# Optimization experiments

Hardware: AMD Instinct MI355X
Metric: run time of the kernel (lower is better)

The kernel has to match this reference:

```python
import jax, jax.numpy as jnp
import numpy as np
import math

B_SZ, T_LEN = 2, 1024
D_MODEL, D_STATE, D_CONV, EXPAND = 1024, 16, 4, 2
D_INNER = EXPAND * D_MODEL            # 2048
DT_RANK = math.ceil(D_MODEL / 16)     # 64


def setup_inputs() -> dict:
    key = jax.random.key(0)
    ks = jax.random.split(key, 10)
    f32 = jnp.float32
    x = jax.random.normal(ks[0], (B_SZ, T_LEN, D_MODEL), f32)
    norm_w = jnp.ones((D_MODEL,), f32)
    in_proj_w = jax.random.normal(ks[1], (2 * D_INNER, D_MODEL), f32) / np.sqrt(D_MODEL)
    conv_w = jax.random.uniform(ks[2], (D_INNER, 1, D_CONV), f32, -0.5, 0.5)
    conv_b = jax.random.uniform(ks[3], (D_INNER,), f32, -0.5, 0.5)
    x_proj_w = jax.random.normal(ks[4], (DT_RANK + 2 * D_STATE, D_INNER), f32) / np.sqrt(D_INNER)
    dt_std = DT_RANK ** (-0.5)
    dt_proj_w = jax.random.uniform(ks[5], (D_INNER, DT_RANK), f32, -dt_std, dt_std)
    # dt bias init: softplus(bias) lands in [dt_min, dt_max]
    dt = jnp.exp(jax.random.uniform(ks[6], (D_INNER,), f32) * (np.log(0.1) - np.log(0.001)) + np.log(0.001))
    dt_proj_b = dt + jnp.log(-jnp.expm1(-dt))
    A_log = jnp.log(jnp.tile(jnp.arange(1, D_STATE + 1, dtype=f32)[None, :], (D_INNER, 1)))
    D_param = jnp.ones((D_INNER,), f32)
    out_proj_w = jax.random.normal(ks[7], (D_MODEL, D_INNER), f32) / np.sqrt(D_INNER)
    return {"x": x, "norm_w": norm_w, "in_proj_w": in_proj_w, "conv_w": conv_w,
            "conv_b": conv_b, "x_proj_w": x_proj_w, "dt_proj_w": dt_proj_w,
            "dt_proj_b": dt_proj_b, "A_log": A_log, "D_param": D_param,
            "out_proj_w": out_proj_w}


def _mamba_forward(x, norm_w, in_proj_w, conv_w, conv_b, x_proj_w,
                   dt_proj_w, dt_proj_b, A_log, D_param, out_proj_w):
    residual = x
    # RMSNorm (torch nn.RMSNorm, eps=None -> finfo eps)
    eps = jnp.finfo(x.dtype).eps
    xn = x * jax.lax.rsqrt(jnp.mean(x * x, axis=-1, keepdims=True) + eps) * norm_w
    # input projection -> ssm stream + gate
    xz = xn @ in_proj_w.T                     # [B,T,2*d_inner]
    x_s, z = xz[..., :D_INNER], xz[..., D_INNER:]
    # causal depthwise conv1d (pad left d_conv-1, matches padding=d_conv-1 then [:T])
    u = jax.lax.conv_general_dilated(
        x_s.transpose(0, 2, 1), conv_w, window_strides=(1,),
        padding=[(D_CONV - 1, 0)], dimension_numbers=("NCH", "OIH", "NCH"),
        feature_group_count=D_INNER) + conv_b[None, :, None]
    u = jax.nn.silu(u).transpose(0, 2, 1)     # [B,T,d_inner]
    # input-dependent SSM params
    x_dbc = u @ x_proj_w.T
    dt_raw = x_dbc[..., :DT_RANK]
    B_ssm = x_dbc[..., DT_RANK:DT_RANK + D_STATE]
    C_ssm = x_dbc[..., DT_RANK + D_STATE:]
    delta = jax.nn.softplus(dt_raw @ dt_proj_w.T + dt_proj_b)   # [B,T,d_inner]
    A = -jnp.exp(A_log)                                         # [d_inner,d_state]
    # discretize
    dA = jnp.exp(jnp.einsum("bti,is->btis", delta, A))          # [B,T,i,s]
    dBu = jnp.einsum("bti,bts->btis", delta * u, B_ssm)         # [B,T,i,s]
    # sequential scan over time (lax.scan, carry h [B,i,s])
    def step(h, inp):
        dA_t, dBu_t, C_t = inp
        h = dA_t * h + dBu_t
        y_t = jnp.einsum("bis,bs->bi", h, C_t)
        return h, y_t
    h0 = jnp.zeros((x.shape[0], D_INNER, D_STATE), x.dtype)
    _, ys = jax.lax.scan(step, h0,
                         (dA.transpose(1, 0, 2, 3), dBu.transpose(1, 0, 2, 3),
                          C_ssm.transpose(1, 0, 2)))
    y = ys.transpose(1, 0, 2) + u * D_param                     # [B,T,d_inner]
    y = y * jax.nn.silu(z)
    return y @ out_proj_w.T + residual


def reference(x, norm_w, in_proj_w, conv_w, conv_b, x_proj_w,
              dt_proj_w, dt_proj_b, A_log, D_param, out_proj_w):
    return _mamba_forward(x, norm_w, in_proj_w, conv_w, conv_b, x_proj_w,
                          dt_proj_w, dt_proj_b, A_log, D_param, out_proj_w)
```

## Files before the change

kernel.cpp:

```cpp
#include <hip/hip_runtime.h>
#include <math.h>

#define B_SZ 2
#define T_LEN 1024
#define D_MODEL 1024
#define D_STATE 16
#define D_INNER 2048
#define DT_RANK 64
#define NTOK (B_SZ * T_LEN)
#define XPROJ_OUT 96
#define XPROJ_LD 128
#define NCHUNK 32
#define CHUNK_L (T_LEN / NCHUNK)
#define NSPLIT 16

typedef __attribute__((ext_vector_type(8))) short bf16x8;
typedef __attribute__((ext_vector_type(4))) float f32x4;

__device__ __forceinline__ float sigmoidf_(float x) { return 1.f / (1.f + __expf(-x)); }

__device__ __forceinline__ unsigned f2bf_u(float f) {
    unsigned u = __float_as_uint(f);
    return (u + 0x7FFFu + ((u >> 16) & 1u)) >> 16;
}
__device__ __forceinline__ float bf2f(unsigned short u) {
    return __uint_as_float((unsigned)u << 16);
}

__device__ __forceinline__ void gload_lds16(const void* g, void* l) {
    __builtin_amdgcn_global_load_lds((const __attribute__((address_space(1))) unsigned*)g,
                                     (__attribute__((address_space(3))) unsigned*)l,
                                     16, 0, 0);
}

__global__ __launch_bounds__(256) void k_prep(const float* __restrict__ x,
                                              const float* __restrict__ norm_w,
                                              const float* __restrict__ w_in,
                                              const float* __restrict__ w_out,
                                              const float* __restrict__ w_x,
                                              const float* __restrict__ w_dt,
                                              unsigned short* __restrict__ xn,
                                              unsigned* __restrict__ wib,
                                              unsigned* __restrict__ wob,
                                              unsigned* __restrict__ wxb,
                                              unsigned* __restrict__ wdtb) {
    __shared__ float red[4];
    int blk = blockIdx.x;
    if (blk < 2048) {
        const float* xr = x + (size_t)blk * D_MODEL;
        int i = threadIdx.x * 4;
        float4 xv = *(const float4*)(xr + i);
        float s = xv.x * xv.x + xv.y * xv.y + xv.z * xv.z + xv.w * xv.w;
#pragma unroll
        for (int m = 1; m <= 32; m <<= 1) s += __shfl_xor(s, m);
        if ((threadIdx.x & 63) == 0) red[threadIdx.x >> 6] = s;
        __syncthreads();
        float tot = red[0] + red[1] + red[2] + red[3];
        float scale = rsqrtf(tot * (1.f / D_MODEL) + 1.1920929e-07f);
        float4 wv = *(const float4*)(norm_w + i);
        uint2 o;
        o.x = f2bf_u(xv.x * scale * wv.x) | (f2bf_u(xv.y * scale * wv.y) << 16);
        o.y = f2bf_u(xv.z * scale * wv.z) | (f2bf_u(xv.w * scale * wv.w) << 16);
        *(uint2*)(xn + (size_t)blk * D_MODEL + i) = o;
        return;
    }
    blk -= 2048;
    const float* src;
    unsigned* dst;
    int lidx;
    if (blk < 2048) {
        src = w_in; dst = wib; lidx = blk * 256 + threadIdx.x;
    } else if (blk < 3072) {
        src = w_out; dst = wob; lidx = (blk - 2048) * 256 + threadIdx.x;
    } else if (blk < 3200) {
        dst = wxb; lidx = (blk - 3072) * 256 + threadIdx.x;
        if (lidx * 8 >= 96 * 2048) {
            uint4 z = {0, 0, 0, 0};
            ((uint4*)dst)[lidx] = z;
            return;
        }
        src = w_x;
    } else {
        src = w_dt; dst = wdtb; lidx = (blk - 3200) * 256 + threadIdx.x;
    }
    float4 a = ((const float4*)src)[lidx * 2];
    float4 b = ((const float4*)src)[lidx * 2 + 1];
    uint4 o;
    o.x = f2bf_u(a.x) | (f2bf_u(a.y) << 16);
    o.y = f2bf_u(a.z) | (f2bf_u(a.w) << 16);
    o.z = f2bf_u(b.x) | (f2bf_u(b.y) << 16);
    o.w = f2bf_u(b.z) | (f2bf_u(b.w) << 16);
    ((uint4*)dst)[lidx] = o;
}


template <int BN, int CW, int EPI>
__global__ __launch_bounds__(256) void gemm_bf16(const unsigned short* __restrict__ A,
                                                 const unsigned short* __restrict__ B,
                                                 void* __restrict__ Cv, int ldc, int K,
                                                 const float* __restrict__ res) {
    constexpr int RW = 4 / CW;
    constexpr int MI = (128 / RW) / 16;
    constexpr int NJ = (BN / CW) / 16;
    __shared__ __align__(16) unsigned short smem[2 * 128 * 64 + 2 * BN * 64];
    unsigned short* As0 = smem;
    unsigned short* Bs0 = smem + 2 * 128 * 64;
    int tid = threadIdx.x;
    int lane = tid & 63, wv = tid >> 6;
    int wr = wv / CW, wc = wv % CW;
    int lm = lane & 15, q = lane >> 4;
    int sw = lm & 7;
    int m0 = blockIdx.x * 128, n0 = blockIdx.y * BN;
    f32x4 acc[MI][NJ] = {};

    auto stage = [&](int bufi, int k0) {
#pragma unroll
        for (int it = 0; it < 4; ++it) {
            int chunk = it * 256 + tid;
            int cc = (chunk & 7) ^ ((chunk >> 3) & 7);
            const unsigned short* g = A + (size_t)(m0 + (chunk >> 3)) * K + k0 + cc * 8;
            char* l = (char*)(As0 + bufi * 128 * 64) + (it * 256 + wv * 64) * 16 + lane * 16;
            gload_lds16(g, l);
        }
#pragma unroll
        for (int it = 0; it < BN / 32; ++it) {
            int chunk = it * 256 + tid;
            int cc = (chunk & 7) ^ ((chunk >> 3) & 7);
            const unsigned short* g = B + (size_t)(n0 + (chunk >> 3)) * K + k0 + cc * 8;
            char* l = (char*)(Bs0 + bufi * BN * 64) + (it * 256 + wv * 64) * 16 + lane * 16;
            gload_lds16(g, l);
        }
    };

    stage(0, 0);
    __syncthreads();
    int cur = 0;
    for (int k0 = 0; k0 < K; k0 += 64) {
        if (k0 + 64 < K) stage(cur ^ 1, k0 + 64);
        const unsigned short* Ac = As0 + cur * 128 * 64;
        const unsigned short* Bc = Bs0 + cur * BN * 64;
#pragma unroll
        for (int h = 0; h < 2; ++h) {
            bf16x8 af[MI], bfr[NJ];
#pragma unroll
            for (int i = 0; i < MI; ++i)
                af[i] = *(const bf16x8*)(Ac + (wr * MI * 16 + i * 16 + lm) * 64 +
                                         (((h << 2) + q) ^ sw) * 8);
#pragma unroll
            for (int j = 0; j < NJ; ++j)
                bfr[j] = *(const bf16x8*)(Bc + (wc * NJ * 16 + j * 16 + lm) * 64 +
                                          (((h << 2) + q) ^ sw) * 8);
#pragma unroll
            for (int i = 0; i < MI; ++i)
#pragma unroll
                for (int j = 0; j < NJ; ++j)
                    acc[i][j] = __builtin_amdgcn_mfma_f32_16x16x32_bf16(af[i], bfr[j], acc[i][j], 0, 0, 0);
        }
        __syncthreads();
        cur ^= 1;
    }
    if (EPI == 0) {
        constexpr int LDT = BN + 8;
        float* Ct = (float*)smem;
#pragma unroll
        for (int i = 0; i < MI; ++i)
#pragma unroll
            for (int j = 0; j < NJ; ++j)
#pragma unroll
                for (int r = 0; r < 4; ++r) {
                    int lr = wr * MI * 16 + i * 16 + q * 4 + r;
                    int lc = wc * NJ * 16 + j * 16 + lm;
                    Ct[lr * LDT + lc] = acc[i][j][r];
                }
        __syncthreads();
        int r0 = tid >> 4, c4 = (tid & 15) * 4;
#pragma unroll
        for (int rr = 0; rr < 8; ++rr) {
            int lr = r0 + rr * 16;
            float4 v = *(float4*)&Ct[lr * LDT + c4];
            float4 rv = *(const float4*)&res[(size_t)(m0 + lr) * ldc + n0 + c4];
            v.x += rv.x; v.y += rv.y; v.z += rv.z; v.w += rv.w;
            *(float4*)&((float*)Cv)[(size_t)(m0 + lr) * ldc + n0 + c4] = v;
        }
    } else {
        constexpr int LDT = BN + 16;
        unsigned short* Ct = smem;
#pragma unroll
        for (int i = 0; i < MI; ++i)
#pragma unroll
            for (int j = 0; j < NJ; ++j)
#pragma unroll
                for (int r = 0; r < 4; ++r) {
                    int lr = wr * MI * 16 + i * 16 + q * 4 + r;
                    int lc = wc * NJ * 16 + j * 16 + lm;
                    float v = acc[i][j][r];
                    if (EPI == 1) {
                        v += res[n0 + lc];
                        v = (v > 20.f) ? v : __logf(1.f + __expf(v));
                    } else {
                        if (n0 >= D_INNER) v = v * sigmoidf_(v);
                    }
                    Ct[lr * LDT + lc] = (unsigned short)f2bf_u(v);
                }
        __syncthreads();
        constexpr int CW8 = BN / 8;
        constexpr int RPP = 256 / CW8;
        int r0 = tid / CW8, cc = (tid % CW8) * 8;
#pragma unroll
        for (int rr = 0; rr < 128 / RPP; ++rr) {
            int lr = r0 + rr * RPP;
            uint4 v = *(uint4*)&Ct[lr * LDT + cc];
            *(uint4*)&((unsigned short*)Cv)[(size_t)(m0 + lr) * ldc + n0 + cc] = v;
        }
    }
}

__global__ __launch_bounds__(256) void xproj_gemm(const unsigned short* __restrict__ A,
                                                  const unsigned short* __restrict__ B,
                                                  unsigned short* __restrict__ part) {
    constexpr int MI = 4, NJ = 4;
    __shared__ __align__(16) unsigned short smem[4 * 128 * 64];
    unsigned short* As0 = smem;
    unsigned short* Bs0 = smem + 2 * 128 * 64;
    int tid = threadIdx.x;
    int lane = tid & 63, wv = tid >> 6;
    int wr = wv >> 1, wc = wv & 1;
    int lm = lane & 15, q = lane >> 4;
    int sw = lm & 7;
    int m0 = blockIdx.x * 128;
    int kbase = blockIdx.y * 128;
    f32x4 acc[MI][NJ] = {};

    auto stage = [&](int bufi, int k0) {
#pragma unroll
        for (int it = 0; it < 4; ++it) {
            int chunk = it * 256 + tid;
            int cc = (chunk & 7) ^ ((chunk >> 3) & 7);
            const unsigned short* g = A + (size_t)(m0 + (chunk >> 3)) * D_INNER + k0 + cc * 8;
            char* l = (char*)(As0 + bufi * 128 * 64) + (it * 256 + wv * 64) * 16 + lane * 16;
            gload_lds16(g, l);
        }
#pragma unroll
        for (int it = 0; it < 4; ++it) {
            int chunk = it * 256 + tid;
            int cc = (chunk & 7) ^ ((chunk >> 3) & 7);
            const unsigned short* g = B + (size_t)(chunk >> 3) * D_INNER + k0 + cc * 8;
            char* l = (char*)(Bs0 + bufi * 128 * 64) + (it * 256 + wv * 64) * 16 + lane * 16;
            gload_lds16(g, l);
        }
    };

    stage(0, kbase);
    __syncthreads();
    for (int ks = 0; ks < 2; ++ks) {
        if (ks == 0) stage(1, kbase + 64);
        const unsigned short* Ac = As0 + ks * 128 * 64;
        const unsigned short* Bc = Bs0 + ks * 128 * 64;
#pragma unroll
        for (int h = 0; h < 2; ++h) {
            bf16x8 af[MI], bfr[NJ];
#pragma unroll
            for (int i = 0; i < MI; ++i)
                af[i] = *(const bf16x8*)(Ac + (wr * 64 + i * 16 + lm) * 64 + (((h << 2) + q) ^ sw) * 8);
#pragma unroll
            for (int j = 0; j < NJ; ++j)
                bfr[j] = *(const bf16x8*)(Bc + (wc * 64 + j * 16 + lm) * 64 + (((h << 2) + q) ^ sw) * 8);
#pragma unroll
            for (int i = 0; i < MI; ++i)
#pragma unroll
                for (int j = 0; j < NJ; ++j)
                    acc[i][j] = __builtin_amdgcn_mfma_f32_16x16x32_bf16(af[i], bfr[j], acc[i][j], 0, 0, 0);
        }
        __syncthreads();
    }
    constexpr int LDT = 144;
    unsigned short* Ct = smem;
#pragma unroll
    for (int i = 0; i < MI; ++i)
#pragma unroll
        for (int j = 0; j < NJ; ++j)
#pragma unroll
            for (int r = 0; r < 4; ++r) {
                int lr = wr * 64 + i * 16 + q * 4 + r;
                int lc = wc * 64 + j * 16 + lm;
                Ct[lr * LDT + lc] = (unsigned short)f2bf_u(acc[i][j][r]);
            }
    __syncthreads();
    unsigned short* dst = part + (size_t)blockIdx.y * (NTOK * XPROJ_LD);
    int r0 = tid >> 4, cc = (tid & 15) * 8;
#pragma unroll
    for (int rr = 0; rr < 8; ++rr) {
        int lr = r0 + rr * 16;
        uint4 v = *(uint4*)&Ct[lr * LDT + cc];
        *(uint4*)&dst[(size_t)(m0 + lr) * XPROJ_LD + cc] = v;
    }
}

__global__ __launch_bounds__(256) void k_xred(const unsigned short* __restrict__ part,
                                              float* __restrict__ dbc,
                                              unsigned short* __restrict__ dtrawb) {
    int idx4 = blockIdx.x * 256 + threadIdx.x;
    float s0 = 0.f, s1 = 0.f, s2 = 0.f, s3 = 0.f;
#pragma unroll
    for (int sp = 0; sp < NSPLIT; ++sp) {
        uint2 v = *(const uint2*)(part + (size_t)sp * (NTOK * XPROJ_LD) + idx4 * 4);
        s0 += __uint_as_float(v.x << 16);
        s1 += __uint_as_float(v.x & 0xFFFF0000u);
        s2 += __uint_as_float(v.y << 16);
        s3 += __uint_as_float(v.y & 0xFFFF0000u);
    }
    float4 sv = {s0, s1, s2, s3};
    *(float4*)(dbc + idx4 * 4) = sv;
    int col = (idx4 * 4) & (XPROJ_LD - 1);
    if (col < DT_RANK) {
        int row = (idx4 * 4) >> 7;
        uint2 o;
        o.x = f2bf_u(s0) | (f2bf_u(s1) << 16);
        o.y = f2bf_u(s2) | (f2bf_u(s3) << 16);
        *(uint2*)(dtrawb + (size_t)row * DT_RANK + col) = o;
    }
}

__global__ __launch_bounds__(256) void k_conv(const unsigned short* __restrict__ xz,
                                              const float* __restrict__ cw,
                                              const float* __restrict__ cb,
                                              unsigned short* __restrict__ ub) {
    int idx = blockIdx.x * 256 + threadIdx.x;
    int c4 = (idx & (D_INNER / 4 - 1)) * 4;
    int t = (idx >> 9) & (T_LEN - 1);
    int b = idx >> 19;
    const unsigned short* xs = xz + (size_t)b * T_LEN * 2 * D_INNER + c4;
    float4 w[4];
#pragma unroll
    for (int i = 0; i < 4; ++i) w[i] = ((const float4*)cw)[c4 + i];
    float4 cbv = *(const float4*)(cb + c4);
    float s[4] = {cbv.x, cbv.y, cbv.z, cbv.w};
#pragma unroll
    for (int k = 0; k < 4; ++k) {
        int tt = t - 3 + k;
        if (tt >= 0) {
            ushort4 xv = *(const ushort4*)(xs + (size_t)tt * 2 * D_INNER);
            float fx0 = bf2f(xv.x), fx1 = bf2f(xv.y), fx2 = bf2f(xv.z), fx3 = bf2f(xv.w);
            float w0 = (k == 0) ? w[0].x : (k == 1) ? w[0].y : (k == 2) ? w[0].z : w[0].w;
            float w1 = (k == 0) ? w[1].x : (k == 1) ? w[1].y : (k == 2) ? w[1].z : w[1].w;
            float w2 = (k == 0) ? w[2].x : (k == 1) ? w[2].y : (k == 2) ? w[2].z : w[2].w;
            float w3 = (k == 0) ? w[3].x : (k == 1) ? w[3].y : (k == 2) ? w[3].z : w[3].w;
            s[0] = fmaf(fx0, w0, s[0]);
            s[1] = fmaf(fx1, w1, s[1]);
            s[2] = fmaf(fx2, w2, s[2]);
            s[3] = fmaf(fx3, w3, s[3]);
        }
    }
    ushort4 o;
    o.x = (unsigned short)f2bf_u(s[0] * sigmoidf_(s[0]));
    o.y = (unsigned short)f2bf_u(s[1] * sigmoidf_(s[1]));
    o.z = (unsigned short)f2bf_u(s[2] * sigmoidf_(s[2]));
    o.w = (unsigned short)f2bf_u(s[3] * sigmoidf_(s[3]));
    *(ushort4*)(ub + (size_t)(b * T_LEN + t) * D_INNER + c4) = o;
}

__global__ __launch_bounds__(256) void k_scan1(const unsigned short* __restrict__ delta,
                                               const unsigned short* __restrict__ ub,
                                               const float* __restrict__ dbc,
                                               const float* __restrict__ A_log,
                                               float* __restrict__ Pbuf,
                                               float* __restrict__ Hbuf) {
    int tid = threadIdx.x;
    int cl = tid >> 2, sq = tid & 3;
    int c0 = blockIdx.x * 64;
    int c = c0 + cl;
    int b = blockIdx.y >> 5, chunk = blockIdx.y & 31;
    int t0 = chunk * CHUNK_L;
    __shared__ float bc[CHUNK_L][32];
    __shared__ __align__(16) unsigned short sd[CHUNK_L][64];
    __shared__ __align__(16) unsigned short su[CHUNK_L][64];
    {
        int t = tid >> 3, col = (tid & 7) * 4;
        const float* src = dbc + ((size_t)b * T_LEN + t0 + t) * XPROJ_LD + DT_RANK + col;
        *(float4*)&bc[t][col] = *(const float4*)src;
    }
    {
        int r = tid >> 3, c8 = (tid & 7) * 8;
        const unsigned short* dp0 = delta + ((size_t)b * T_LEN + t0) * D_INNER + c0;
        const unsigned short* up0 = ub + ((size_t)b * T_LEN + t0) * D_INNER + c0;
        *(uint4*)&sd[r][c8] = *(const uint4*)(dp0 + (size_t)r * D_INNER + c8);
        *(uint4*)&su[r][c8] = *(const uint4*)(up0 + (size_t)r * D_INNER + c8);
    }
    __syncthreads();
    float4 av = *(const float4*)(A_log + (size_t)c * D_STATE + sq * 4);
    float A0 = -__expf(av.x), A1 = -__expf(av.y), A2 = -__expf(av.z), A3 = -__expf(av.w);
    float h0 = 0.f, h1 = 0.f, h2 = 0.f, h3 = 0.f, sumd = 0.f;
#pragma unroll 4
    for (int t = 0; t < CHUNK_L; ++t) {
        float dv = bf2f(sd[t][cl]);
        float uv = bf2f(su[t][cl]);
        float du = dv * uv;
        sumd += dv;
        float4 Bv = *(const float4*)&bc[t][sq * 4];
        h0 = fmaf(__expf(dv * A0), h0, du * Bv.x);
        h1 = fmaf(__expf(dv * A1), h1, du * Bv.y);
        h2 = fmaf(__expf(dv * A2), h2, du * Bv.z);
        h3 = fmaf(__expf(dv * A3), h3, du * Bv.w);
    }
    size_t o = ((size_t)((b * NCHUNK + chunk) * D_INNER) + c) * 16 + sq * 4;
    float4 hv = {h0, h1, h2, h3};
    *(float4*)(Hbuf + o) = hv;
    float4 pv = {__expf(A0 * sumd), __expf(A1 * sumd), __expf(A2 * sumd), __expf(A3 * sumd)};
    *(float4*)(Pbuf + o) = pv;
}

__global__ __launch_bounds__(256) void k_scan2(const float* __restrict__ Pbuf,
                                               const float* __restrict__ Hbuf,
                                               float* __restrict__ Sbuf) {
    int idx = blockIdx.x * 256 + threadIdx.x;
    int b = idx >> 15, r = idx & 32767;
    size_t base = (size_t)b * NCHUNK * (D_INNER * 16) + r;
    float p[NCHUNK], hl[NCHUNK];
#pragma unroll
    for (int ch = 0; ch < NCHUNK; ++ch) {
        size_t o = base + (size_t)ch * (D_INNER * 16);
        p[ch] = Pbuf[o];
        hl[ch] = Hbuf[o];
    }
    float h = 0.f;
#pragma unroll
    for (int ch = 0; ch < NCHUNK; ++ch) {
        Sbuf[base + (size_t)ch * (D_INNER * 16)] = h;
        h = fmaf(p[ch], h, hl[ch]);
    }
}

__global__ __launch_bounds__(256) void k_scan3(const unsigned short* __restrict__ delta,
                                               const unsigned short* __restrict__ ub,
                                               const float* __restrict__ dbc,
                                               const unsigned short* __restrict__ xz,
                                               const float* __restrict__ A_log,
                                               const float* __restrict__ Dp,
                                               const float* __restrict__ Sbuf,
                                               unsigned short* __restrict__ yb) {
    int tid = threadIdx.x;
    int cl = tid >> 2, sq = tid & 3;
    int c0 = blockIdx.x * 64;
    int c = c0 + cl;
    int b = blockIdx.y >> 5, chunk = blockIdx.y & 31;
    int t0 = chunk * CHUNK_L;
    __shared__ float bc[CHUNK_L][32];
    __shared__ __align__(16) unsigned short sd[CHUNK_L][64];
    __shared__ __align__(16) unsigned short su[CHUNK_L][64];
    __shared__ __align__(16) unsigned short szy[CHUNK_L][64];
    {
        int t = tid >> 3, col = (tid & 7) * 4;
        const float* src = dbc + ((size_t)b * T_LEN + t0 + t) * XPROJ_LD + DT_RANK + col;
        *(float4*)&bc[t][col] = *(const float4*)src;
    }
    int r = tid >> 3, c8 = (tid & 7) * 8;
    {
        const unsigned short* dp0 = delta + ((size_t)b * T_LEN + t0) * D_INNER + c0;
        const unsigned short* up0 = ub + ((size_t)b * T_LEN + t0) * D_INNER + c0;
        const unsigned short* zp0 = xz + ((size_t)b * T_LEN + t0) * 2 * D_INNER + D_INNER + c0;
        *(uint4*)&sd[r][c8] = *(const uint4*)(dp0 + (size_t)r * D_INNER + c8);
        *(uint4*)&su[r][c8] = *(const uint4*)(up0 + (size_t)r * D_INNER + c8);
        *(uint4*)&szy[r][c8] = *(const uint4*)(zp0 + (size_t)r * 2 * D_INNER + c8);
    }
    __syncthreads();
    float4 av = *(const float4*)(A_log + (size_t)c * D_STATE + sq * 4);
    float A0 = -__expf(av.x), A1 = -__expf(av.y), A2 = -__expf(av.z), A3 = -__expf(av.w);
    float Dc = Dp[c];
    size_t ho = ((size_t)((b * NCHUNK + chunk) * D_INNER) + c) * 16 + sq * 4;
    float4 hv = *(const float4*)(Sbuf + ho);
    float h0 = hv.x, h1 = hv.y, h2 = hv.z, h3 = hv.w;
#pragma unroll 2
    for (int t = 0; t < CHUNK_L; ++t) {
        float dv = bf2f(sd[t][cl]);
        float uv = bf2f(su[t][cl]);
        float du = dv * uv;
        float4 Bv = *(const float4*)&bc[t][sq * 4];
        float4 Cv = *(const float4*)&bc[t][16 + sq * 4];
        h0 = fmaf(__expf(dv * A0), h0, du * Bv.x);
        h1 = fmaf(__expf(dv * A1), h1, du * Bv.y);
        h2 = fmaf(__expf(dv * A2), h2, du * Bv.z);
        h3 = fmaf(__expf(dv * A3), h3, du * Bv.w);
        float yp = h0 * Cv.x + h1 * Cv.y + h2 * Cv.z + h3 * Cv.w;
        yp += __shfl_xor(yp, 1);
        yp += __shfl_xor(yp, 2);
        if (sq == 0) {
            float sz = bf2f(szy[t][cl]);
            szy[t][cl] = (unsigned short)f2bf_u((yp + Dc * uv) * sz);
        }
    }
    __syncthreads();
    {
        unsigned short* yp0 = yb + ((size_t)b * T_LEN + t0) * D_INNER + c0;
        *(uint4*)(yp0 + (size_t)r * D_INNER + c8) = *(uint4*)&szy[r][c8];
    }
}

extern "C" void kernel_launch(void* const* d_in, const int* in_sizes, int n_in,
                              void* d_out, int out_size, void* d_ws, size_t ws_size,
                              hipStream_t stream) {
    const float* x         = (const float*)d_in[0];
    const float* norm_w    = (const float*)d_in[1];
    const float* in_proj_w = (const float*)d_in[2];
    const float* conv_w    = (const float*)d_in[3];
    const float* conv_b    = (const float*)d_in[4];
    const float* x_proj_w  = (const float*)d_in[5];
    const float* dt_proj_w = (const float*)d_in[6];
    const float* dt_proj_b = (const float*)d_in[7];
    const float* A_log     = (const float*)d_in[8];
    const float* D_param   = (const float*)d_in[9];
    const float* out_proj_w= (const float*)d_in[10];
    float* out = (float*)d_out;

    float* ws = (float*)d_ws;
    unsigned short* xzb    = (unsigned short*)(ws);
    unsigned short* ub     = (unsigned short*)(ws + 4194304);
    unsigned short* yb     = (unsigned short*)(ws + 6291456);
    unsigned short* partb  = (unsigned short*)(ws + 8388608);
    float*          dbc    = ws + 12582912;
    unsigned short* deltab = (unsigned short*)(ws + 12845056);
    float*          Pbuf   = ws + 14942208;
    float*          Hbuf   = ws + 17039360;
    float*          Sbuf   = ws + 19136512;
    unsigned short* wib    = (unsigned short*)(ws + 21233664);
    unsigned short* wob    = (unsigned short*)(ws + 23330816);
    unsigned short* wxb    = (unsigned short*)(ws + 24379392);
    unsigned short* wdtb   = (unsigned short*)(ws + 24510464);
    unsigned short* dtrawb = (unsigned short*)(ws + 24576000);
    unsigned short* xnb    = (unsigned short*)(ws + 24641536);

    k_prep<<<5312, 256, 0, stream>>>(x, norm_w, in_proj_w, out_proj_w, x_proj_w, dt_proj_w,
                                     xnb, (unsigned*)wib, (unsigned*)wob, (unsigned*)wxb,
                                     (unsigned*)wdtb);
    gemm_bf16<128, 2, 3><<<dim3(NTOK / 128, 4096 / 128), 256, 0, stream>>>(
        xnb, wib, xzb, 2 * D_INNER, D_MODEL, nullptr);
    k_conv<<<(NTOK * D_INNER / 4) / 256, 256, 0, stream>>>(xzb, conv_w, conv_b, ub);
    xproj_gemm<<<dim3(NTOK / 128, NSPLIT), 256, 0, stream>>>(ub, wxb, partb);
    k_xred<<<(NTOK * XPROJ_LD) / 1024, 256, 0, stream>>>(partb, dbc, dtrawb);
    gemm_bf16<64, 1, 1><<<dim3(NTOK / 128, D_INNER / 64), 256, 0, stream>>>(
        dtrawb, wdtb, deltab, D_INNER, DT_RANK, dt_proj_b);
    k_scan1<<<dim3(D_INNER / 64, B_SZ * NCHUNK), 256, 0, stream>>>(deltab, ub, dbc, A_log,
                                                                   Pbuf, Hbuf);
    k_scan2<<<(B_SZ * D_INNER * D_STATE) / 256, 256, 0, stream>>>(Pbuf, Hbuf, Sbuf);
    k_scan3<<<dim3(D_INNER / 64, B_SZ * NCHUNK), 256, 0, stream>>>(deltab, ub, dbc, xzb, A_log,
                                                                   D_param, Sbuf, yb);
    gemm_bf16<64, 2, 0><<<dim3(NTOK / 128, D_MODEL / 64), 256, 0, stream>>>(
        yb, wob, (void*)out, D_MODEL, D_INNER, x);

    (void)in_sizes; (void)n_in; (void)out_size; (void)ws_size;
}
```

Baseline: 218.3 us.

## Fold inter-chunk state scan into scan3 and use 64x64 tiles for out-proj

Removes the separate k_scan2 kernel. Each scan3 block now serially combines the prior chunks' decay and state buffers to rebuild its starting state, which saves a launch and the Sbuf round trip but adds redundant O(chunk) global reads per block. It also replaces the 128x64 out-projection GEMM with a dedicated 64x64-tile kernel. That doubles the grid to improve CU occupancy for the small output GEMM, at the cost of less operand reuse per tile.

```diff
diff --git a/kernel.cpp b/kernel.cpp
--- a/kernel.cpp
+++ b/kernel.cpp
@@ -159,30 +159,7 @@
         __syncthreads();
         cur ^= 1;
     }
-    if (EPI == 0) {
-        constexpr int LDT = BN + 8;
-        float* Ct = (float*)smem;
-#pragma unroll
-        for (int i = 0; i < MI; ++i)
-#pragma unroll
-            for (int j = 0; j < NJ; ++j)
-#pragma unroll
-                for (int r = 0; r < 4; ++r) {
-                    int lr = wr * MI * 16 + i * 16 + q * 4 + r;
-                    int lc = wc * NJ * 16 + j * 16 + lm;
-                    Ct[lr * LDT + lc] = acc[i][j][r];
-                }
-        __syncthreads();
-        int r0 = tid >> 4, c4 = (tid & 15) * 4;
-#pragma unroll
-        for (int rr = 0; rr < 8; ++rr) {
-            int lr = r0 + rr * 16;
-            float4 v = *(float4*)&Ct[lr * LDT + c4];
-            float4 rv = *(const float4*)&res[(size_t)(m0 + lr) * ldc + n0 + c4];
-            v.x += rv.x; v.y += rv.y; v.z += rv.z; v.w += rv.w;
-            *(float4*)&((float*)Cv)[(size_t)(m0 + lr) * ldc + n0 + c4] = v;
-        }
-    } else {
+    {
         constexpr int LDT = BN + 16;
         unsigned short* Ct = smem;
 #pragma unroll
@@ -212,6 +189,91 @@
             uint4 v = *(uint4*)&Ct[lr * LDT + cc];
             *(uint4*)&((unsigned short*)Cv)[(size_t)(m0 + lr) * ldc + n0 + cc] = v;
         }
+    }
+}
+
+__global__ __launch_bounds__(256) void gemm_out64(const unsigned short* __restrict__ A,
+                                                  const unsigned short* __restrict__ B,
+                                                  float* __restrict__ C, int ldc, int K,
+                                                  const float* __restrict__ res) {
+    __shared__ __align__(16) unsigned short smem[4 * 64 * 64];
+    unsigned short* As0 = smem;
+    unsigned short* Bs0 = smem + 2 * 64 * 64;
+    int tid = threadIdx.x;
+    int lane = tid & 63, wv = tid >> 6;
+    int wr = wv >> 1, wc = wv & 1;
+    int lm = lane & 15, q = lane >> 4;
+    int sw = lm & 7;
+    int m0 = blockIdx.x * 64, n0 = blockIdx.y * 64;
+    f32x4 acc[2][2] = {};
+
+    auto stage = [&](int bufi, int k0) {
+#pragma unroll
+        for (int it = 0; it < 2; ++it) {
+            int chunk = it * 256 + tid;
+            int cc = (chunk & 7) ^ ((chunk >> 3) & 7);
+            const unsigned short* g = A + (size_t)(m0 + (chunk >> 3)) * K + k0 + cc * 8;
+            char* l = (char*)(As0 + bufi * 64 * 64) + (it * 256 + wv * 64) * 16 + lane * 16;
+            gload_lds16(g, l);
+        }
+#pragma unroll
+        for (int it = 0; it < 2; ++it) {
+            int chunk = it * 256 + tid;
+            int cc = (chunk & 7) ^ ((chunk >> 3) & 7);
+            const unsigned short* g = B + (size_t)(n0 + (chunk >> 3)) * K + k0 + cc * 8;
+            char* l = (char*)(Bs0 + bufi * 64 * 64) + (it * 256 + wv * 64) * 16 + lane * 16;
+            gload_lds16(g, l);
+        }
+    };
+
+    stage(0, 0);
+    __syncthreads();
+    int cur = 0;
+    for (int k0 = 0; k0 < K; k0 += 64) {
+        if (k0 + 64 < K) stage(cur ^ 1, k0 + 64);
+        const unsigned short* Ac = As0 + cur * 64 * 64;
+        const unsigned short* Bc = Bs0 + cur * 64 * 64;
+#pragma unroll
+        for (int h = 0; h < 2; ++h) {
+            bf16x8 af[2], bfr[2];
+#pragma unroll
+            for (int i = 0; i < 2; ++i)
+                af[i] = *(const bf16x8*)(Ac + (wr * 32 + i * 16 + lm) * 64 +
+                                         (((h << 2) + q) ^ sw) * 8);
+#pragma unroll
+            for (int j = 0; j < 2; ++j)
+                bfr[j] = *(const bf16x8*)(Bc + (wc * 32 + j * 16 + lm) * 64 +
+                                          (((h << 2) + q) ^ sw) * 8);
+#pragma unroll
+            for (int i = 0; i < 2; ++i)
+#pragma unroll
+                for (int j = 0; j < 2; ++j)
+                    acc[i][j] = __builtin_amdgcn_mfma_f32_16x16x32_bf16(af[i], bfr[j], acc[i][j], 0, 0, 0);
+        }
+        __syncthreads();
+        cur ^= 1;
+    }
+    constexpr int LDT = 72;
+    float* Ct = (float*)smem;
+#pragma unroll
+    for (int i = 0; i < 2; ++i)
+#pragma unroll
+        for (int j = 0; j < 2; ++j)
+#pragma unroll
+            for (int r = 0; r < 4; ++r) {
+                int lr = wr * 32 + i * 16 + q * 4 + r;
+                int lc = wc * 32 + j * 16 + lm;
+                Ct[lr * LDT + lc] = acc[i][j][r];
+            }
+    __syncthreads();
+    int r0 = tid >> 4, c4 = (tid & 15) * 4;
+#pragma unroll
+    for (int rr = 0; rr < 4; ++rr) {
+        int lr = r0 + rr * 16;
+        float4 v = *(float4*)&Ct[lr * LDT + c4];
+        float4 rv = *(const float4*)&res[(size_t)(m0 + lr) * ldc + n0 + c4];
+        v.x += rv.x; v.y += rv.y; v.z += rv.z; v.w += rv.w;
+        *(float4*)&C[(size_t)(m0 + lr) * ldc + n0 + c4] = v;
     }
 }
 
@@ -409,34 +471,14 @@
     *(float4*)(Pbuf + o) = pv;
 }
 
-__global__ __launch_bounds__(256) void k_scan2(const float* __restrict__ Pbuf,
-                                               const float* __restrict__ Hbuf,
-                                               float* __restrict__ Sbuf) {
-    int idx = blockIdx.x * 256 + threadIdx.x;
-    int b = idx >> 15, r = idx & 32767;
-    size_t base = (size_t)b * NCHUNK * (D_INNER * 16) + r;
-    float p[NCHUNK], hl[NCHUNK];
-#pragma unroll
-    for (int ch = 0; ch < NCHUNK; ++ch) {
-        size_t o = base + (size_t)ch * (D_INNER * 16);
-        p[ch] = Pbuf[o];
-        hl[ch] = Hbuf[o];
-    }
-    float h = 0.f;
-#pragma unroll
-    for (int ch = 0; ch < NCHUNK; ++ch) {
-        Sbuf[base + (size_t)ch * (D_INNER * 16)] = h;
-        h = fmaf(p[ch], h, hl[ch]);
-    }
-}
-
 __global__ __launch_bounds__(256) void k_scan3(const unsigned short* __restrict__ delta,
                                                const unsigned short* __restrict__ ub,
                                                const float* __restrict__ dbc,
                                                const unsigned short* __restrict__ xz,
                                                const float* __restrict__ A_log,
                                                const float* __restrict__ Dp,
-                                               const float* __restrict__ Sbuf,
+                                               const float* __restrict__ Pbuf,
+                                               const float* __restrict__ Hbuf,
                                                unsigned short* __restrict__ yb) {
     int tid = threadIdx.x;
     int cl = tid >> 2, sq = tid & 3;
@@ -462,13 +504,23 @@
         *(uint4*)&su[r][c8] = *(const uint4*)(up0 + (size_t)r * D_INNER + c8);
         *(uint4*)&szy[r][c8] = *(const uint4*)(zp0 + (size_t)r * 2 * D_INNER + c8);
     }
+    float h0 = 0.f, h1 = 0.f, h2 = 0.f, h3 = 0.f;
+    {
+        size_t sbase = ((size_t)(b * NCHUNK) * D_INNER + c) * 16 + sq * 4;
+        for (int ch = 0; ch < chunk; ++ch) {
+            size_t o = sbase + (size_t)ch * ((size_t)D_INNER * 16);
+            float4 pv = *(const float4*)(Pbuf + o);
+            float4 hlv = *(const float4*)(Hbuf + o);
+            h0 = fmaf(pv.x, h0, hlv.x);
+            h1 = fmaf(pv.y, h1, hlv.y);
+            h2 = fmaf(pv.z, h2, hlv.z);
+            h3 = fmaf(pv.w, h3, hlv.w);
+        }
+    }
     __syncthreads();
     float4 av = *(const float4*)(A_log + (size_t)c * D_STATE + sq * 4);
     float A0 = -__expf(av.x), A1 = -__expf(av.y), A2 = -__expf(av.z), A3 = -__expf(av.w);
     float Dc = Dp[c];
-    size_t ho = ((size_t)((b * NCHUNK + chunk) * D_INNER) + c) * 16 + sq * 4;
-    float4 hv = *(const float4*)(Sbuf + ho);
-    float h0 = hv.x, h1 = hv.y, h2 = hv.z, h3 = hv.w;
 #pragma unroll 2
     for (int t = 0; t < CHUNK_L; ++t) {
         float dv = bf2f(sd[t][cl]);
@@ -520,7 +572,6 @@
     unsigned short* deltab = (unsigned short*)(ws + 12845056);
     float*          Pbuf   = ws + 14942208;
     float*          Hbuf   = ws + 17039360;
-    float*          Sbuf   = ws + 19136512;
     unsigned short* wib    = (unsigned short*)(ws + 21233664);
     unsigned short* wob    = (unsigned short*)(ws + 23330816);
     unsigned short* wxb    = (unsigned short*)(ws + 24379392);
@@ -540,11 +591,10 @@
         dtrawb, wdtb, deltab, D_INNER, DT_RANK, dt_proj_b);
     k_scan1<<<dim3(D_INNER / 64, B_SZ * NCHUNK), 256, 0, stream>>>(deltab, ub, dbc, A_log,
                                                                    Pbuf, Hbuf);
-    k_scan2<<<(B_SZ * D_INNER * D_STATE) / 256, 256, 0, stream>>>(Pbuf, Hbuf, Sbuf);
     k_scan3<<<dim3(D_INNER / 64, B_SZ * NCHUNK), 256, 0, stream>>>(deltab, ub, dbc, xzb, A_log,
-                                                                   D_param, Sbuf, yb);
-    gemm_bf16<64, 2, 0><<<dim3(NTOK / 128, D_MODEL / 64), 256, 0, stream>>>(
-        yb, wob, (void*)out, D_MODEL, D_INNER, x);
+                                                                   D_param, Pbuf, Hbuf, yb);
+    gemm_out64<<<dim3(NTOK / 64, D_MODEL / 64), 256, 0, stream>>>(
+        yb, wob, out, D_MODEL, D_INNER, x);
 
     (void)in_sizes; (void)n_in; (void)out_size; (void)ws_size;
 }
```

Measured after the change: 220.4 us. About the same (+0.9%).
